# Optimization experiments

Hardware: AMD Instinct MI355X
Metric: run time of the kernel (lower is better)

## Reference

```python
import math
import jax, jax.numpy as jnp
import numpy as np

B, T, E, H = 4, 4096, 512, 8
D = E // H
TOP_K = int(3 * math.log(T))  # autocorrelation_factor * log(time_length) = 24


def setup_inputs() -> dict:
    key = jax.random.key(0)
    ks = jax.random.split(key, 9)
    s = 0.02
    return {
        "hidden_states": jax.random.normal(ks[0], (B, T, E), jnp.float32),
        "Wq": jax.random.normal(ks[1], (E, E), jnp.float32) * s,
        "bq": jax.random.normal(ks[2], (E,), jnp.float32) * s,
        "Wk": jax.random.normal(ks[3], (E, E), jnp.float32) * s,
        "bk": jax.random.normal(ks[4], (E,), jnp.float32) * s,
        "Wv": jax.random.normal(ks[5], (E, E), jnp.float32) * s,
        "bv": jax.random.normal(ks[6], (E,), jnp.float32) * s,
        "Wo": jax.random.normal(ks[7], (E, E), jnp.float32) * s,
        "bo": jax.random.normal(ks[8], (E,), jnp.float32) * s,
    }


def _heads(x):
    # [B,T,E] -> [B*H,T,D] (b-major over heads, matching torch view/transpose/reshape)
    return x.reshape(B, T, H, D).transpose(0, 2, 1, 3).reshape(B * H, T, D)


def reference(hidden_states, Wq, bq, Wk, bk, Wv, bv, Wo, bo):
    q = _heads(hidden_states @ Wq.T + bq)
    k = _heads(hidden_states @ Wk.T + bk)
    v = _heads(hidden_states @ Wv.T + bv)

    # FFT-based autocorrelation: irfft(rfft(q) * conj(rfft(k)))  -> [B*H,T,D]
    qf = jnp.fft.rfft(q, n=T, axis=1)
    kf = jnp.fft.rfft(k, n=T, axis=1)
    ac = jnp.fft.irfft(qf * jnp.conj(kf), n=T, axis=1)

    # mean over heads and channels -> [B,T]; eval-mode per-batch top-k delays
    ac_mean = ac.reshape(B, H, T, D).mean(axis=(1, 3))
    top_vals, top_idx = jax.lax.top_k(ac_mean, TOP_K)      # [B,K]
    w = jax.nn.softmax(top_vals, axis=-1)                  # [B,K]

    # torch .repeat(num_heads,...) tiles batch entries: row j uses batch j % B
    w_t = jnp.tile(w, (H, 1))        # [B*H,K]
    d_t = jnp.tile(top_idx, (H, 1))  # [B*H,K]

    t = jnp.arange(T)
    agg = jnp.zeros_like(v)
    for i in range(TOP_K):
        idx = (t[None, :] + d_t[:, i:i + 1]) % T           # circular shift by -delay
        rolled = jnp.take_along_axis(v, idx[:, :, None], axis=1)
        agg = agg + w_t[:, i][:, None, None] * rolled

    out = agg.reshape(B, H, T, D).transpose(0, 2, 1, 3).reshape(B, T, E)
    return out @ Wo.T + bo
```

## Files before the change

kernel.cpp:

```cpp
#include <hip/hip_runtime.h>
#include <math.h>

#define B_ 4
#define T_ 4096
#define E_ 512
#define H_ 8
#define TOPK 24
#define FH 2049
#define FHP 2064

typedef __attribute__((ext_vector_type(8))) short bf16x8;
typedef __attribute__((ext_vector_type(4))) float f32x4;

__device__ __forceinline__ unsigned short f2bf(float f) {
    unsigned u = __float_as_uint(f);
    u = (u + 0x7FFFu + ((u >> 16) & 1u)) >> 16;
    return (unsigned short)u;
}
__device__ __forceinline__ float bf2f(unsigned short h) {
    return __uint_as_float(((unsigned)h) << 16);
}

__global__ __launch_bounds__(256) void split_hidden(const float* __restrict__ x,
                                                    unsigned short* __restrict__ hi,
                                                    unsigned short* __restrict__ lo)
{
    int i = (blockIdx.x * 256 + threadIdx.x) * 4;
    float4 v = *(const float4*)&x[i];
    float f[4] = {v.x, v.y, v.z, v.w};
    unsigned short hh[4], ll[4];
#pragma unroll
    for (int j = 0; j < 4; j++) {
        hh[j] = f2bf(f[j]);
        ll[j] = f2bf(f[j] - bf2f(hh[j]));
    }
    *(ushort4*)&hi[i] = make_ushort4(hh[0], hh[1], hh[2], hh[3]);
    *(ushort4*)&lo[i] = make_ushort4(ll[0], ll[1], ll[2], ll[3]);
}

__global__ __launch_bounds__(256) void split_w4(const float* __restrict__ w0,
                                                const float* __restrict__ w1,
                                                const float* __restrict__ w2,
                                                const float* __restrict__ w3,
                                                unsigned short* __restrict__ hi,
                                                unsigned short* __restrict__ lo)
{
    const float* src = (blockIdx.y == 0) ? w0 : (blockIdx.y == 1) ? w1
                     : (blockIdx.y == 2) ? w2 : w3;
    size_t off = (size_t)blockIdx.y * (E_ * E_);
    int i = (blockIdx.x * 256 + threadIdx.x) * 4;
    float4 v = *(const float4*)&src[i];
    float f[4] = {v.x, v.y, v.z, v.w};
    unsigned short hh[4], ll[4];
#pragma unroll
    for (int j = 0; j < 4; j++) {
        hh[j] = f2bf(f[j]);
        ll[j] = f2bf(f[j] - bf2f(hh[j]));
    }
    *(ushort4*)&hi[off + i] = make_ushort4(hh[0], hh[1], hh[2], hh[3]);
    *(ushort4*)&lo[off + i] = make_ushort4(ll[0], ll[1], ll[2], ll[3]);
}

template<int PASSES, int OMODE>
__global__ __launch_bounds__(256) void mfma_gemm(const unsigned short* __restrict__ Ah,
                                                 const unsigned short* __restrict__ Al,
                                                 const unsigned short* __restrict__ Bh,
                                                 const unsigned short* __restrict__ Bl,
                                                 const float* __restrict__ bias,
                                                 const float* __restrict__ bias2,
                                                 void* __restrict__ Cp)
{
    constexpr int NT = (PASSES == 3) ? 4 : 2;
    constexpr int TSZ = 128 * 40;
    __shared__ short smem[NT * TSZ];
    const int tid = threadIdx.x;
    const int m0 = blockIdx.x * 128;
    const int n0 = blockIdx.y * 128;
    const int wid = tid >> 6, lane = tid & 63;
    const int wn = wid >> 1, wm = wid & 1;
    const int lr = lane & 15, lg = lane >> 4;
    const int kb = lg * 8;

    short* At  = smem;
    short* Alt = smem + ((PASSES == 3) ? TSZ : 0);
    short* Bt  = smem + ((PASSES == 3) ? 2 : 1) * TSZ;
    short* Blt = smem + ((PASSES == 3) ? 3 : 1) * TSZ;

    f32x4 acc[4][4];
#pragma unroll
    for (int i = 0; i < 4; i++)
#pragma unroll
        for (int j = 0; j < 4; j++) acc[i][j] = (f32x4)0.f;

    const int c0 = tid, c1 = tid + 256;
    const int r0 = c0 >> 2, kp0 = (c0 & 3) << 3;
    const int r1 = c1 >> 2, kp1 = (c1 & 3) << 3;

    for (int k0 = 0; k0 < 512; k0 += 32) {
        __syncthreads();
        *(bf16x8*)&At[r0 * 40 + kp0] = *(const bf16x8*)&Ah[(size_t)(n0 + r0) * 512 + k0 + kp0];
        *(bf16x8*)&At[r1 * 40 + kp1] = *(const bf16x8*)&Ah[(size_t)(n0 + r1) * 512 + k0 + kp1];
        *(bf16x8*)&Bt[r0 * 40 + kp0] = *(const bf16x8*)&Bh[(size_t)(m0 + r0) * 512 + k0 + kp0];
        *(bf16x8*)&Bt[r1 * 40 + kp1] = *(const bf16x8*)&Bh[(size_t)(m0 + r1) * 512 + k0 + kp1];
        if (PASSES == 3) {
            *(bf16x8*)&Alt[r0 * 40 + kp0] = *(const bf16x8*)&Al[(size_t)(n0 + r0) * 512 + k0 + kp0];
            *(bf16x8*)&Alt[r1 * 40 + kp1] = *(const bf16x8*)&Al[(size_t)(n0 + r1) * 512 + k0 + kp1];
            *(bf16x8*)&Blt[r0 * 40 + kp0] = *(const bf16x8*)&Bl[(size_t)(m0 + r0) * 512 + k0 + kp0];
            *(bf16x8*)&Blt[r1 * 40 + kp1] = *(const bf16x8*)&Bl[(size_t)(m0 + r1) * 512 + k0 + kp1];
        }
        __syncthreads();
        bf16x8 a[4], b[4];
#pragma unroll
        for (int f = 0; f < 4; f++) {
            a[f] = *(bf16x8*)&At[(wn * 64 + f * 16 + lr) * 40 + kb];
            b[f] = *(bf16x8*)&Bt[(wm * 64 + f * 16 + lr) * 40 + kb];
        }
        if (PASSES == 3) {
            bf16x8 a2[4], b2[4];
#pragma unroll
            for (int f = 0; f < 4; f++) {
                a2[f] = *(bf16x8*)&Alt[(wn * 64 + f * 16 + lr) * 40 + kb];
                b2[f] = *(bf16x8*)&Blt[(wm * 64 + f * 16 + lr) * 40 + kb];
            }
#pragma unroll
            for (int i = 0; i < 4; i++)
#pragma unroll
                for (int j = 0; j < 4; j++) {
                    acc[i][j] = __builtin_amdgcn_mfma_f32_16x16x32_bf16(a[i], b[j], acc[i][j], 0, 0, 0);
                    acc[i][j] = __builtin_amdgcn_mfma_f32_16x16x32_bf16(a[i], b2[j], acc[i][j], 0, 0, 0);
                    acc[i][j] = __builtin_amdgcn_mfma_f32_16x16x32_bf16(a2[i], b[j], acc[i][j], 0, 0, 0);
                }
        } else {
#pragma unroll
            for (int i = 0; i < 4; i++)
#pragma unroll
                for (int j = 0; j < 4; j++)
                    acc[i][j] = __builtin_amdgcn_mfma_f32_16x16x32_bf16(a[i], b[j], acc[i][j], 0, 0, 0);
        }
    }

    const float* bp = (m0 >= 512) ? bias2 : bias;
    const int mb = m0 & 511;
    float bs[4];
#pragma unroll
    for (int j = 0; j < 4; j++) bs[j] = bp[mb + wm * 64 + j * 16 + lr];

    if (OMODE == 1) {
        float* C = (float*)Cp;
        const int qk = m0 >> 9;
        const int bidx = n0 >> 12;
        const int t0 = (n0 & 4095) + wn * 64;
#pragma unroll
        for (int i = 0; i < 4; i++)
#pragma unroll
            for (int j = 0; j < 4; j++) {
                int t = t0 + i * 16 + lg * 4;
                int e = mb + wm * 64 + j * 16 + lr;
                size_t row = (size_t)(qk * 2048 + bidx * 512 + e);
                float4 o = make_float4(acc[i][j][0] + bs[j], acc[i][j][1] + bs[j],
                                       acc[i][j][2] + bs[j], acc[i][j][3] + bs[j]);
                *(float4*)&C[row * 4096 + t] = o;
            }
    } else if (OMODE == 0) {
        float* C = (float*)Cp;
#pragma unroll
        for (int i = 0; i < 4; i++)
#pragma unroll
            for (int j = 0; j < 4; j++) {
                int m = m0 + wm * 64 + j * 16 + lr;
#pragma unroll
                for (int r = 0; r < 4; r++) {
                    int n = n0 + wn * 64 + i * 16 + lg * 4 + r;
                    C[(size_t)n * 512 + m] = acc[i][j][r] + bs[j];
                }
            }
    } else {
        unsigned short* C = (unsigned short*)Cp;
#pragma unroll
        for (int i = 0; i < 4; i++)
#pragma unroll
            for (int j = 0; j < 4; j++) {
                int m = m0 + wm * 64 + j * 16 + lr;
#pragma unroll
                for (int r = 0; r < 4; r++) {
                    int n = n0 + wn * 64 + i * 16 + lg * 4 + r;
                    C[(size_t)n * 512 + m] = f2bf(acc[i][j][r] + bs[j]);
                }
            }
    }
}

template<int SGN>
__device__ __forceinline__ void radix8(float* xr, float* xi)
{
    const float C = 0.70710678118654752440f;
    const float S = (float)SGN;
    float t0r = xr[0] + xr[4], t0i = xi[0] + xi[4];
    float t1r = xr[1] + xr[5], t1i = xi[1] + xi[5];
    float t2r = xr[2] + xr[6], t2i = xi[2] + xi[6];
    float t3r = xr[3] + xr[7], t3i = xi[3] + xi[7];
    float u0r = xr[0] - xr[4], u0i = xi[0] - xi[4];
    float a1r = xr[1] - xr[5], a1i = xi[1] - xi[5];
    float a2r = xr[2] - xr[6], a2i = xi[2] - xi[6];
    float a3r = xr[3] - xr[7], a3i = xi[3] - xi[7];
    float u1r = C * (a1r - S * a1i), u1i = C * (S * a1r + a1i);
    float u2r = -S * a2i,            u2i = S * a2r;
    float u3r = -C * (a3r + S * a3i), u3i = C * (S * a3r - a3i);
    float v0r = t0r + t2r, v0i = t0i + t2i;
    float w0r = t0r - t2r, w0i = t0i - t2i;
    float v1r = t1r + t3r, v1i = t1i + t3i;
    float w1r = -S * (t1i - t3i), w1i = S * (t1r - t3r);
    float p0r = u0r + u2r, p0i = u0i + u2i;
    float q0r = u0r - u2r, q0i = u0i - u2i;
    float p1r = u1r + u3r, p1i = u1i + u3i;
    float q1r = -S * (u1i - u3i), q1i = S * (u1r - u3r);
    xr[0] = v0r + v1r; xi[0] = v0i + v1i;
    xr[4] = v0r - v1r; xi[4] = v0i - v1i;
    xr[2] = w0r + w1r; xi[2] = w0i + w1i;
    xr[6] = w0r - w1r; xi[6] = w0i - w1i;
    xr[1] = p0r + p1r; xi[1] = p0i + p1i;
    xr[5] = p0r - p1r; xi[5] = p0i - p1i;
    xr[3] = q0r + q1r; xi[3] = q0i + q1i;
    xr[7] = q0r - q1r; xi[7] = q0i - q1i;
}

__device__ __forceinline__ void twmul(float& xr, float& xi, float wc, float ws)
{
    float a = xr, b = xi;
    xr = a * wc - b * ws;
    xi = a * ws + b * wc;
}

__device__ __forceinline__ void twiddle7(float* xr, float* xi, int n, float ang)
{
    float s1, c1;
    __sincosf(ang * (float)n, &s1, &c1);
    float wc = c1, ws = s1;
    twmul(xr[1], xi[1], wc, ws);
#pragma unroll
    for (int r = 2; r < 8; r++) {
        float nc = wc * c1 - ws * s1;
        float ns = wc * s1 + ws * c1;
        wc = nc; ws = ns;
        twmul(xr[r], xi[r], wc, ws);
    }
}

#define SW(i) ((i) + ((i) >> 3))

template<int SGN>
__device__ __forceinline__ void fft_core(float* xr, float* xi,
                                         float* lre, float* lim, int tid)
{
    const float TW = (float)SGN * 6.28318530717958647693f;
    __syncthreads();
    radix8<SGN>(xr, xi);
    twiddle7(xr, xi, tid, TW / 4096.f);
#pragma unroll
    for (int r = 0; r < 8; r++) {
        int idx = r * 512 + tid;
        lre[SW(idx)] = xr[r]; lim[SW(idx)] = xi[r];
    }
    __syncthreads();
    const int b2 = (tid >> 6) * 512, n2 = tid & 63;
#pragma unroll
    for (int s = 0; s < 8; s++) {
        int idx = b2 + n2 + s * 64;
        xr[s] = lre[SW(idx)]; xi[s] = lim[SW(idx)];
    }
    __syncthreads();
    radix8<SGN>(xr, xi);
    twiddle7(xr, xi, n2, TW / 512.f);
#pragma unroll
    for (int r = 0; r < 8; r++) {
        int idx = b2 + r * 64 + n2;
        lre[SW(idx)] = xr[r]; lim[SW(idx)] = xi[r];
    }
    __syncthreads();
    const int b3 = (tid >> 3) * 64, n3 = tid & 7;
#pragma unroll
    for (int s = 0; s < 8; s++) {
        int idx = b3 + n3 + s * 8;
        xr[s] = lre[SW(idx)]; xi[s] = lim[SW(idx)];
    }
    __syncthreads();
    radix8<SGN>(xr, xi);
    twiddle7(xr, xi, n3, TW / 64.f);
#pragma unroll
    for (int r = 0; r < 8; r++) {
        int idx = b3 + r * 8 + n3;
        lre[SW(idx)] = xr[r]; lim[SW(idx)] = xi[r];
    }
    __syncthreads();
#pragma unroll
    for (int s = 0; s < 8; s++) {
        int idx = tid * 8 + s;
        xr[s] = lre[SW(idx)]; xi[s] = lim[SW(idx)];
    }
    __syncthreads();
    radix8<SGN>(xr, xi);
    const int fr = ((tid & 7) << 6) | (((tid >> 3) & 7) << 3) | (tid >> 6);
#pragma unroll
    for (int r = 0; r < 8; r++) {
        int f = r * 512 + fr;
        lre[SW(f)] = xr[r]; lim[SW(f)] = xi[r];
    }
    __syncthreads();
}

__global__ __launch_bounds__(512) void fft_fwd_kernel(const float* __restrict__ Qt,
                                                      const float* __restrict__ Kt,
                                                      float2* __restrict__ prodp)
{
    __shared__ float lre[4608];
    __shared__ float lim[4608];
    const int bid = blockIdx.x;
    const int tid = threadIdx.x;
    const int b = bid >> 7, chunk = bid & 127;
    float par[5] = {0.f, 0.f, 0.f, 0.f, 0.f};
    float pai[4] = {0.f, 0.f, 0.f, 0.f};
    for (int c = 0; c < 4; c++) {
        const int e = chunk * 4 + c;
        const float* q = Qt + ((size_t)(b * 512 + e)) * 4096;
        const float* k = Kt + ((size_t)(b * 512 + e)) * 4096;
        float xr[8], xi[8];
#pragma unroll
        for (int s = 0; s < 8; s++) {
            xr[s] = q[tid + 512 * s];
            xi[s] = k[tid + 512 * s];
        }
        fft_core<-1>(xr, xi, lre, lim, tid);
#pragma unroll
        for (int s = 0; s < 4; s++) {
            int f = tid + 512 * s;
            int nf = (4096 - f) & 4095;
            float Ax = lre[SW(f)],  Ay = lim[SW(f)];
            float Bx = lre[SW(nf)], By = lim[SW(nf)];
            float qx = 0.5f * (Ax + Bx), qy = 0.5f * (Ay - By);
            float kx = 0.5f * (Ay + By), ky = -0.5f * (Ax - Bx);
            par[s] += qx * kx + qy * ky;
            pai[s] += qy * kx - qx * ky;
        }
        if (tid == 0) {
            float Ax = lre[SW(2048)], Ay = lim[SW(2048)];
            par[4] += Ax * Ay;
        }
    }
    float2* out = prodp + (size_t)bid * FHP;
#pragma unroll
    for (int s = 0; s < 4; s++)
        out[tid + 512 * s] = make_float2(par[s], pai[s]);
    if (tid == 0) out[2048] = make_float2(par[4], 0.f);
}

__global__ __launch_bounds__(256) void reduce_s(const float2* __restrict__ prodp,
                                                float2* __restrict__ S)
{
    const int f = blockIdx.x * 256 + threadIdx.x;
    const int b = blockIdx.y;
    if (f >= FH) return;
    float sx = 0.f, sy = 0.f;
    const float2* p = prodp + (size_t)(b * 128) * FHP + f;
#pragma unroll 8
    for (int j = 0; j < 128; j++) {
        float2 v = p[(size_t)j * FHP];
        sx += v.x; sy += v.y;
    }
    S[b * FHP + f] = make_float2(sx, sy);
}

__global__ __launch_bounds__(512) void ifft_kernel(const float2* __restrict__ S,
                                                   float* __restrict__ acm)
{
    __shared__ float lre[4608];
    __shared__ float lim[4608];
    const int b = blockIdx.x, tid = threadIdx.x;
    float xr[8], xi[8];
#pragma unroll
    for (int s = 0; s < 8; s++) {
        int idx = tid + 512 * s;
        if (idx <= 2048) {
            float2 v = S[b * FHP + idx];
            xr[s] = v.x; xi[s] = v.y;
        } else {
            float2 v = S[b * FHP + (4096 - idx)];
            xr[s] = v.x; xi[s] = -v.y;
        }
    }
    fft_core<1>(xr, xi, lre, lim, tid);
    const float scale = 1.0f / ((float)T_ * (float)E_);
#pragma unroll
    for (int s = 0; s < 8; s++) {
        int p = tid + 512 * s;
        acm[b * T_ + p] = lre[SW(p)] * scale;
    }
}

__global__ __launch_bounds__(256) void topk_kernel(const float* __restrict__ acm,
                                                   int* __restrict__ delays,
                                                   float* __restrict__ weights)
{
    __shared__ float vals[4096];
    __shared__ float bv[256];
    __shared__ int   bi[256];
    __shared__ float topv[TOPK];
    const int b = blockIdx.x, tid = threadIdx.x;
#pragma unroll
    for (int s = 0; s < 16; s++) vals[tid + 256 * s] = acm[b * T_ + tid + 256 * s];
    __syncthreads();
    for (int it = 0; it < TOPK; it++) {
        float best = -INFINITY; int bidx = 0;
#pragma unroll
        for (int s = 0; s < 16; s++) {
            int idx = tid * 16 + s;
            float v = vals[idx];
            if (v > best) { best = v; bidx = idx; }
        }
        bv[tid] = best; bi[tid] = bidx;
        __syncthreads();
        for (int off = 128; off > 0; off >>= 1) {
            if (tid < off) {
                if (bv[tid + off] > bv[tid] ||
                    (bv[tid + off] == bv[tid] && bi[tid + off] < bi[tid])) {
                    bv[tid] = bv[tid + off]; bi[tid] = bi[tid + off];
                }
            }
            __syncthreads();
        }
        if (tid == 0) {
            delays[b * TOPK + it] = bi[0];
            topv[it] = bv[0];
            vals[bi[0]] = -INFINITY;
        }
        __syncthreads();
    }
    if (tid == 0) {
        float mx = topv[0];
        float w[TOPK], sum = 0.f;
        for (int i = 0; i < TOPK; i++) { w[i] = expf(topv[i] - mx); sum += w[i]; }
        for (int i = 0; i < TOPK; i++) weights[b * TOPK + i] = w[i] / sum;
    }
}

__global__ __launch_bounds__(256) void agg_kernel(const unsigned short* __restrict__ V,
                                                  const int* __restrict__ delays,
                                                  const float* __restrict__ wts,
                                                  unsigned short* __restrict__ agg)
{
    __shared__ int   dly[B_][TOPK];
    __shared__ float wt[B_][TOPK];
    const int tid = threadIdx.x, b = blockIdx.y;
    if (tid < B_ * TOPK) {
        dly[tid / TOPK][tid % TOPK] = delays[tid];
        wt[tid / TOPK][tid % TOPK]  = wts[tid];
    }
    __syncthreads();
    const int lane = tid & 63, w = tid >> 6;
    const int t = blockIdx.x * 4 + w;
    const int e8 = lane * 8;
    const int h = e8 >> 6;
    const int c = (b * H_ + h) % B_;
    const unsigned short* Vb = V + (size_t)b * T_ * E_;
    float acc[8];
#pragma unroll
    for (int j = 0; j < 8; j++) acc[j] = 0.f;
#pragma unroll
    for (int i = 0; i < TOPK; i++) {
        int tt = (t + dly[c][i]) & (T_ - 1);
        bf16x8 v = *(const bf16x8*)&Vb[(size_t)tt * E_ + e8];
        float wg = wt[c][i];
#pragma unroll
        for (int j = 0; j < 8; j++)
            acc[j] += wg * bf2f((unsigned short)v[j]);
    }
    bf16x8 o;
#pragma unroll
    for (int j = 0; j < 8; j++) o[j] = (short)f2bf(acc[j]);
    *(bf16x8*)&agg[((size_t)b * T_ + t) * E_ + e8] = o;
}

extern "C" void kernel_launch(void* const* d_in, const int* in_sizes, int n_in,
                              void* d_out, int out_size, void* d_ws, size_t ws_size,
                              hipStream_t stream)
{
    const float* hidden = (const float*)d_in[0];
    const float* Wq = (const float*)d_in[1]; const float* bq = (const float*)d_in[2];
    const float* Wk = (const float*)d_in[3]; const float* bk = (const float*)d_in[4];
    const float* Wv = (const float*)d_in[5]; const float* bv = (const float*)d_in[6];
    const float* Wo = (const float*)d_in[7]; const float* bo = (const float*)d_in[8];

    char* ws = (char*)d_ws;
    const size_t QT_OFF  = 0;
    const size_t KT_OFF  = 33554432;
    const size_t VB_OFF  = 67108864;
    const size_t BIG_OFF = 83886080;
    const size_t BIG2_OFF= 100663296;
    const size_t WHI_OFF = 117702656;
    const size_t WLO_OFF = 119799808;
    const size_t S_OFF   = 121896960;
    const size_t ACM_OFF = 121963008;
    const size_t DEL_OFF = 122028544;
    const size_t WTS_OFF = 122028928;
    if (ws_size < 122029312) return;

    float*  Qt   = (float*)(ws + QT_OFF);
    unsigned short* Vb  = (unsigned short*)(ws + VB_OFF);
    unsigned short* Ah  = (unsigned short*)(ws + BIG_OFF);
    unsigned short* Al  = (unsigned short*)(ws + BIG2_OFF);
    float2* prodp = (float2*)(ws + BIG_OFF);
    unsigned short* Ag  = (unsigned short*)(ws + BIG2_OFF);
    unsigned short* Whi = (unsigned short*)(ws + WHI_OFF);
    unsigned short* Wlo = (unsigned short*)(ws + WLO_OFF);
    float2* S    = (float2*)(ws + S_OFF);
    float*  acm  = (float*)(ws + ACM_OFF);
    int*    delays = (int*)(ws + DEL_OFF);
    float*  wts    = (float*)(ws + WTS_OFF);

    unsigned short* Wvh = Whi + 2 * 262144;
    unsigned short* Woh = Whi + 3 * 262144;

    split_hidden<<<8192, 256, 0, stream>>>(hidden, Ah, Al);
    dim3 wg(256, 4);
    split_w4<<<wg, 256, 0, stream>>>(Wq, Wk, Wv, Wo, Whi, Wlo);

    dim3 gqk(8, 128);
    mfma_gemm<3, 1><<<gqk, 256, 0, stream>>>(Ah, Al, Whi, Wlo, bq, bk, Qt);
    dim3 gv(4, 128);
    mfma_gemm<1, 2><<<gv, 256, 0, stream>>>(Ah, Ah, Wvh, Wvh, bv, bv, Vb);

    fft_fwd_kernel<<<512, 512, 0, stream>>>(Qt, (float*)(ws + KT_OFF), prodp);
    dim3 rg((FH + 255) / 256, B_);
    reduce_s<<<rg, 256, 0, stream>>>(prodp, S);
    ifft_kernel<<<B_, 512, 0, stream>>>(S, acm);
    topk_kernel<<<B_, 256, 0, stream>>>(acm, delays, wts);

    dim3 ag(T_ / 4, B_);
    agg_kernel<<<ag, 256, 0, stream>>>(Vb, delays, wts, Ag);
    mfma_gemm<1, 0><<<gv, 256, 0, stream>>>(Ag, Ag, Woh, Woh, bo, bo, (float*)d_out);
}
```

Baseline: 231.3 us.

## FFT hidden states directly and fold Wq/Wk into one precomputed bilinear matrix

The Q and K projections followed by two FFTs are replaced by one FFT of the transposed hidden states (linearity). The cross-spectrum sum is then computed as a bilinear form using M = Wq^T·Wk, which is formed per call and split into bf16 hi/lo parts. A 3-pass split-bf16 MFMA GEMM produces Y = Z·M, and a dot kernel reduces Y against Z per frequency. The q/k biases are dropped, since they only change the DC bin and so only add a constant to the autocorrelation, which top-k and softmax ignore. This removes the 1024-wide QK projection, halves the number of FFT rows and cuts the fp32 workspace traffic, at the cost of a new transpose kernel, the M-prep GEMM and extra bf16 split error on the spectra.

```diff
diff --git a/kernel.cpp b/kernel.cpp
--- a/kernel.cpp
+++ b/kernel.cpp
@@ -8,6 +8,8 @@
 #define TOPK 24
 #define FH 2049
 #define FHP 2064
+#define F2 2064
+#define ZROWS 16512
 
 typedef __attribute__((ext_vector_type(8))) short bf16x8;
 typedef __attribute__((ext_vector_type(4))) float f32x4;
@@ -21,53 +23,110 @@
     return __uint_as_float(((unsigned)h) << 16);
 }
 
-__global__ __launch_bounds__(256) void split_hidden(const float* __restrict__ x,
-                                                    unsigned short* __restrict__ hi,
-                                                    unsigned short* __restrict__ lo)
-{
-    int i = (blockIdx.x * 256 + threadIdx.x) * 4;
-    float4 v = *(const float4*)&x[i];
-    float f[4] = {v.x, v.y, v.z, v.w};
-    unsigned short hh[4], ll[4];
-#pragma unroll
-    for (int j = 0; j < 4; j++) {
-        hh[j] = f2bf(f[j]);
-        ll[j] = f2bf(f[j] - bf2f(hh[j]));
-    }
-    *(ushort4*)&hi[i] = make_ushort4(hh[0], hh[1], hh[2], hh[3]);
-    *(ushort4*)&lo[i] = make_ushort4(ll[0], ll[1], ll[2], ll[3]);
-}
-
-__global__ __launch_bounds__(256) void split_w4(const float* __restrict__ w0,
-                                                const float* __restrict__ w1,
-                                                const float* __restrict__ w2,
-                                                const float* __restrict__ w3,
-                                                unsigned short* __restrict__ hi,
-                                                unsigned short* __restrict__ lo)
-{
-    const float* src = (blockIdx.y == 0) ? w0 : (blockIdx.y == 1) ? w1
-                     : (blockIdx.y == 2) ? w2 : w3;
-    size_t off = (size_t)blockIdx.y * (E_ * E_);
+__global__ __launch_bounds__(256) void trsp_split(const float* __restrict__ hid,
+                                                  float* __restrict__ Htr,
+                                                  unsigned short* __restrict__ Ah)
+{
+    __shared__ float tile[64][68];
+    const int b = blockIdx.z;
+    const int t0 = blockIdx.x * 64, e0 = blockIdx.y * 64;
+    const int r = threadIdx.x >> 4;
+    const int c4 = (threadIdx.x & 15) * 4;
+#pragma unroll
+    for (int s = 0; s < 4; s++) {
+        int t = t0 + r + 16 * s;
+        float4 v = *(const float4*)&hid[((size_t)b * T_ + t) * E_ + e0 + c4];
+        tile[r + 16 * s][c4 + 0] = v.x; tile[r + 16 * s][c4 + 1] = v.y;
+        tile[r + 16 * s][c4 + 2] = v.z; tile[r + 16 * s][c4 + 3] = v.w;
+        ushort4 hv = make_ushort4(f2bf(v.x), f2bf(v.y), f2bf(v.z), f2bf(v.w));
+        *(ushort4*)&Ah[((size_t)b * T_ + t) * E_ + e0 + c4] = hv;
+    }
+    __syncthreads();
+#pragma unroll
+    for (int s = 0; s < 4; s++) {
+        int e = e0 + r + 16 * s;
+        float4 o;
+        o.x = tile[c4 + 0][r + 16 * s];
+        o.y = tile[c4 + 1][r + 16 * s];
+        o.z = tile[c4 + 2][r + 16 * s];
+        o.w = tile[c4 + 3][r + 16 * s];
+        *(float4*)&Htr[((size_t)b * E_ + e) * T_ + t0 + c4] = o;
+    }
+}
+
+__global__ __launch_bounds__(256) void split_w2(const float* __restrict__ wv,
+                                                const float* __restrict__ wo,
+                                                unsigned short* __restrict__ Wvh,
+                                                unsigned short* __restrict__ Woh)
+{
+    const float* src = blockIdx.y ? wo : wv;
+    unsigned short* dst = blockIdx.y ? Woh : Wvh;
     int i = (blockIdx.x * 256 + threadIdx.x) * 4;
     float4 v = *(const float4*)&src[i];
-    float f[4] = {v.x, v.y, v.z, v.w};
-    unsigned short hh[4], ll[4];
-#pragma unroll
-    for (int j = 0; j < 4; j++) {
-        hh[j] = f2bf(f[j]);
-        ll[j] = f2bf(f[j] - bf2f(hh[j]));
-    }
-    *(ushort4*)&hi[off + i] = make_ushort4(hh[0], hh[1], hh[2], hh[3]);
-    *(ushort4*)&lo[off + i] = make_ushort4(ll[0], ll[1], ll[2], ll[3]);
-}
-
-template<int PASSES, int OMODE>
+    *(ushort4*)&dst[i] = make_ushort4(f2bf(v.x), f2bf(v.y), f2bf(v.z), f2bf(v.w));
+}
+
+__global__ __launch_bounds__(256) void wprep_m(const float* __restrict__ Wq,
+                                               const float* __restrict__ Wk,
+                                               unsigned short* __restrict__ Mth,
+                                               unsigned short* __restrict__ Mtl)
+{
+    __shared__ float As[8][132];
+    __shared__ float Bs[8][132];
+    const int j0 = blockIdx.x * 128, k0 = blockIdx.y * 128;
+    const int tid = threadIdx.x;
+    const int tm = tid & 15, tn = tid >> 4;
+    const int le = tid >> 5, lc = (tid & 31) * 4;
+    float acc[8][8];
+#pragma unroll
+    for (int i = 0; i < 8; i++)
+#pragma unroll
+        for (int j = 0; j < 8; j++) acc[i][j] = 0.f;
+    for (int eb = 0; eb < 512; eb += 8) {
+        __syncthreads();
+        *(float4*)&As[le][lc] = *(const float4*)&Wq[((size_t)(eb + le)) * 512 + k0 + lc];
+        *(float4*)&Bs[le][lc] = *(const float4*)&Wk[((size_t)(eb + le)) * 512 + j0 + lc];
+        __syncthreads();
+#pragma unroll
+        for (int e = 0; e < 8; e++) {
+            float a[8], bb[8];
+            *(float4*)&a[0] = *(float4*)&As[e][4 * tn];
+            *(float4*)&a[4] = *(float4*)&As[e][64 + 4 * tn];
+            *(float4*)&bb[0] = *(float4*)&Bs[e][4 * tm];
+            *(float4*)&bb[4] = *(float4*)&Bs[e][64 + 4 * tm];
+#pragma unroll
+            for (int i = 0; i < 8; i++)
+#pragma unroll
+                for (int j = 0; j < 8; j++)
+                    acc[i][j] += a[i] * bb[j];
+        }
+    }
+#pragma unroll
+    for (int jj = 0; jj < 8; jj++) {
+        int j = j0 + ((jj < 4) ? (4 * tm + jj) : (64 + 4 * tm + jj - 4));
+        ushort4 h0, l0, h1, l1;
+        float v0[4] = {acc[0][jj], acc[1][jj], acc[2][jj], acc[3][jj]};
+        float v1[4] = {acc[4][jj], acc[5][jj], acc[6][jj], acc[7][jj]};
+        unsigned short hh[4], ll[4];
+#pragma unroll
+        for (int r = 0; r < 4; r++) { hh[r] = f2bf(v0[r]); ll[r] = f2bf(v0[r] - bf2f(hh[r])); }
+        h0 = make_ushort4(hh[0], hh[1], hh[2], hh[3]); l0 = make_ushort4(ll[0], ll[1], ll[2], ll[3]);
+#pragma unroll
+        for (int r = 0; r < 4; r++) { hh[r] = f2bf(v1[r]); ll[r] = f2bf(v1[r] - bf2f(hh[r])); }
+        h1 = make_ushort4(hh[0], hh[1], hh[2], hh[3]); l1 = make_ushort4(ll[0], ll[1], ll[2], ll[3]);
+        *(ushort4*)&Mth[(size_t)j * 512 + k0 + 4 * tn] = h0;
+        *(ushort4*)&Mtl[(size_t)j * 512 + k0 + 4 * tn] = l0;
+        *(ushort4*)&Mth[(size_t)j * 512 + k0 + 64 + 4 * tn] = h1;
+        *(ushort4*)&Mtl[(size_t)j * 512 + k0 + 64 + 4 * tn] = l1;
+    }
+}
+
+template<int PASSES, int AMODE, int OMODE, int HASBIAS>
 __global__ __launch_bounds__(256) void mfma_gemm(const unsigned short* __restrict__ Ah,
                                                  const unsigned short* __restrict__ Al,
                                                  const unsigned short* __restrict__ Bh,
                                                  const unsigned short* __restrict__ Bl,
                                                  const float* __restrict__ bias,
-                                                 const float* __restrict__ bias2,
                                                  void* __restrict__ Cp)
 {
     constexpr int NT = (PASSES == 3) ? 4 : 2;
@@ -92,19 +151,26 @@
 #pragma unroll
         for (int j = 0; j < 4; j++) acc[i][j] = (f32x4)0.f;
 
-    const int c0 = tid, c1 = tid + 256;
-    const int r0 = c0 >> 2, kp0 = (c0 & 3) << 3;
-    const int r1 = c1 >> 2, kp1 = (c1 & 3) << 3;
+    const int r0 = tid >> 2, kp0 = (tid & 3) << 3;
+    const int r1 = (tid + 256) >> 2, kp1 = ((tid + 256) & 3) << 3;
 
     for (int k0 = 0; k0 < 512; k0 += 32) {
         __syncthreads();
-        *(bf16x8*)&At[r0 * 40 + kp0] = *(const bf16x8*)&Ah[(size_t)(n0 + r0) * 512 + k0 + kp0];
-        *(bf16x8*)&At[r1 * 40 + kp1] = *(const bf16x8*)&Ah[(size_t)(n0 + r1) * 512 + k0 + kp1];
+        size_t a0, a1;
+        if (AMODE == 0) {
+            a0 = (size_t)(n0 + r0) * 512 + k0 + kp0;
+            a1 = (size_t)(n0 + r1) * 512 + k0 + kp1;
+        } else {
+            a0 = ((size_t)((k0 + kp0) >> 3) * ZROWS + n0 + r0) * 8;
+            a1 = ((size_t)((k0 + kp1) >> 3) * ZROWS + n0 + r1) * 8;
+        }
+        *(bf16x8*)&At[r0 * 40 + kp0] = *(const bf16x8*)&Ah[a0];
+        *(bf16x8*)&At[r1 * 40 + kp1] = *(const bf16x8*)&Ah[a1];
         *(bf16x8*)&Bt[r0 * 40 + kp0] = *(const bf16x8*)&Bh[(size_t)(m0 + r0) * 512 + k0 + kp0];
         *(bf16x8*)&Bt[r1 * 40 + kp1] = *(const bf16x8*)&Bh[(size_t)(m0 + r1) * 512 + k0 + kp1];
         if (PASSES == 3) {
-            *(bf16x8*)&Alt[r0 * 40 + kp0] = *(const bf16x8*)&Al[(size_t)(n0 + r0) * 512 + k0 + kp0];
-            *(bf16x8*)&Alt[r1 * 40 + kp1] = *(const bf16x8*)&Al[(size_t)(n0 + r1) * 512 + k0 + kp1];
+            *(bf16x8*)&Alt[r0 * 40 + kp0] = *(const bf16x8*)&Al[a0];
+            *(bf16x8*)&Alt[r1 * 40 + kp1] = *(const bf16x8*)&Al[a1];
             *(bf16x8*)&Blt[r0 * 40 + kp0] = *(const bf16x8*)&Bl[(size_t)(m0 + r0) * 512 + k0 + kp0];
             *(bf16x8*)&Blt[r1 * 40 + kp1] = *(const bf16x8*)&Bl[(size_t)(m0 + r1) * 512 + k0 + kp1];
         }
@@ -139,29 +205,11 @@
         }
     }
 
-    const float* bp = (m0 >= 512) ? bias2 : bias;
-    const int mb = m0 & 511;
     float bs[4];
 #pragma unroll
-    for (int j = 0; j < 4; j++) bs[j] = bp[mb + wm * 64 + j * 16 + lr];
-
-    if (OMODE == 1) {
-        float* C = (float*)Cp;
-        const int qk = m0 >> 9;
-        const int bidx = n0 >> 12;
-        const int t0 = (n0 & 4095) + wn * 64;
-#pragma unroll
-        for (int i = 0; i < 4; i++)
-#pragma unroll
-            for (int j = 0; j < 4; j++) {
-                int t = t0 + i * 16 + lg * 4;
-                int e = mb + wm * 64 + j * 16 + lr;
-                size_t row = (size_t)(qk * 2048 + bidx * 512 + e);
-                float4 o = make_float4(acc[i][j][0] + bs[j], acc[i][j][1] + bs[j],
-                                       acc[i][j][2] + bs[j], acc[i][j][3] + bs[j]);
-                *(float4*)&C[row * 4096 + t] = o;
-            }
-    } else if (OMODE == 0) {
+    for (int j = 0; j < 4; j++) bs[j] = HASBIAS ? bias[m0 + wm * 64 + j * 16 + lr] : 0.f;
+
+    if (OMODE == 0) {
         float* C = (float*)Cp;
 #pragma unroll
         for (int i = 0; i < 4; i++)
@@ -204,7 +252,7 @@
     float a2r = xr[2] - xr[6], a2i = xi[2] - xi[6];
     float a3r = xr[3] - xr[7], a3i = xi[3] - xi[7];
     float u1r = C * (a1r - S * a1i), u1i = C * (S * a1r + a1i);
-    float u2r = -S * a2i,            u2i = S * a2r;
+    float u2r = -S * a2i,             u2i = S * a2r;
     float u3r = -C * (a3r + S * a3i), u3i = C * (S * a3r - a3i);
     float v0r = t0r + t2r, v0i = t0i + t2i;
     float w0r = t0r - t2r, w0i = t0i - t2i;
@@ -308,26 +356,26 @@
     __syncthreads();
 }
 
-__global__ __launch_bounds__(512) void fft_fwd_kernel(const float* __restrict__ Qt,
-                                                      const float* __restrict__ Kt,
-                                                      float2* __restrict__ prodp)
+__global__ __launch_bounds__(512) void fft_fwd_z(const float* __restrict__ Htr,
+                                                 unsigned short* __restrict__ Zh,
+                                                 unsigned short* __restrict__ Zl)
 {
     __shared__ float lre[4608];
     __shared__ float lim[4608];
     const int bid = blockIdx.x;
     const int tid = threadIdx.x;
-    const int b = bid >> 7, chunk = bid & 127;
-    float par[5] = {0.f, 0.f, 0.f, 0.f, 0.f};
-    float pai[4] = {0.f, 0.f, 0.f, 0.f};
-    for (int c = 0; c < 4; c++) {
-        const int e = chunk * 4 + c;
-        const float* q = Qt + ((size_t)(b * 512 + e)) * 4096;
-        const float* k = Kt + ((size_t)(b * 512 + e)) * 4096;
+    const int b = bid >> 6, g = bid & 63;
+    const int e0 = g * 8;
+    unsigned uh[4][2][4], ul[4][2][4];
+#pragma unroll
+    for (int p = 0; p < 4; p++) {
+        const float* he = Htr + ((size_t)(b * 512 + e0 + 2 * p)) * 4096;
+        const float* ho = Htr + ((size_t)(b * 512 + e0 + 2 * p + 1)) * 4096;
         float xr[8], xi[8];
 #pragma unroll
         for (int s = 0; s < 8; s++) {
-            xr[s] = q[tid + 512 * s];
-            xi[s] = k[tid + 512 * s];
+            xr[s] = he[tid + 512 * s];
+            xi[s] = ho[tid + 512 * s];
         }
         fft_core<-1>(xr, xi, lre, lim, tid);
 #pragma unroll
@@ -338,35 +386,79 @@
             float Bx = lre[SW(nf)], By = lim[SW(nf)];
             float qx = 0.5f * (Ax + Bx), qy = 0.5f * (Ay - By);
             float kx = 0.5f * (Ay + By), ky = -0.5f * (Ax - Bx);
-            par[s] += qx * kx + qy * ky;
-            pai[s] += qy * kx - qx * ky;
+            unsigned short h0 = f2bf(qx), h1 = f2bf(kx);
+            unsigned short l0 = f2bf(qx - bf2f(h0)), l1 = f2bf(kx - bf2f(h1));
+            uh[s][0][p] = (unsigned)h0 | ((unsigned)h1 << 16);
+            ul[s][0][p] = (unsigned)l0 | ((unsigned)l1 << 16);
+            unsigned short h2 = f2bf(qy), h3 = f2bf(ky);
+            unsigned short l2 = f2bf(qy - bf2f(h2)), l3 = f2bf(ky - bf2f(h3));
+            uh[s][1][p] = (unsigned)h2 | ((unsigned)h3 << 16);
+            ul[s][1][p] = (unsigned)l2 | ((unsigned)l3 << 16);
         }
         if (tid == 0) {
             float Ax = lre[SW(2048)], Ay = lim[SW(2048)];
-            par[4] += Ax * Ay;
-        }
-    }
-    float2* out = prodp + (size_t)bid * FHP;
+            size_t r2048 = ((size_t)b * F2 + 2048) * 2;
+            size_t base0 = ((size_t)g * ZROWS + r2048) * 8 + 2 * p;
+            unsigned short h = f2bf(Ax);
+            Zh[base0] = h; Zl[base0] = f2bf(Ax - bf2f(h));
+            unsigned short h2 = f2bf(Ay);
+            Zh[base0 + 1] = h2; Zl[base0 + 1] = f2bf(Ay - bf2f(h2));
+            size_t base1 = ((size_t)g * ZROWS + r2048 + 1) * 8 + 2 * p;
+            Zh[base1] = 0; Zl[base1] = 0;
+            Zh[base1 + 1] = 0; Zl[base1 + 1] = 0;
+        }
+    }
 #pragma unroll
     for (int s = 0; s < 4; s++)
-        out[tid + 512 * s] = make_float2(par[s], pai[s]);
-    if (tid == 0) out[2048] = make_float2(par[4], 0.f);
-}
-
-__global__ __launch_bounds__(256) void reduce_s(const float2* __restrict__ prodp,
-                                                float2* __restrict__ S)
-{
-    const int f = blockIdx.x * 256 + threadIdx.x;
+#pragma unroll
+        for (int c = 0; c < 2; c++) {
+            size_t row = ((size_t)b * F2 + tid + 512 * s) * 2 + c;
+            size_t off = ((size_t)g * ZROWS + row) * 8;
+            bf16x8 vh, vl;
+#pragma unroll
+            for (int p = 0; p < 4; p++) {
+                vh[2 * p]     = (short)(uh[s][c][p] & 0xffff);
+                vh[2 * p + 1] = (short)(uh[s][c][p] >> 16);
+                vl[2 * p]     = (short)(ul[s][c][p] & 0xffff);
+                vl[2 * p + 1] = (short)(ul[s][c][p] >> 16);
+            }
+            *(bf16x8*)&Zh[off] = vh;
+            *(bf16x8*)&Zl[off] = vl;
+        }
+}
+
+__global__ __launch_bounds__(256) void dot_s(const float* __restrict__ Y,
+                                             const unsigned short* __restrict__ Zh,
+                                             const unsigned short* __restrict__ Zl,
+                                             float2* __restrict__ S)
+{
+    const int lane = threadIdx.x & 63, w = threadIdx.x >> 6;
+    const int f = blockIdx.x * 256 + w * 64 + lane;
     const int b = blockIdx.y;
-    if (f >= FH) return;
-    float sx = 0.f, sy = 0.f;
-    const float2* p = prodp + (size_t)(b * 128) * FHP + f;
-#pragma unroll 8
-    for (int j = 0; j < 128; j++) {
-        float2 v = p[(size_t)j * FHP];
-        sx += v.x; sy += v.y;
-    }
-    S[b * FHP + f] = make_float2(sx, sy);
+    if (f > 2048) return;
+    const size_t row = ((size_t)b * F2 + f) * 2;
+    float sre = 0.f, sim = 0.f;
+    for (int g = 0; g < 64; g++) {
+        size_t zoff = ((size_t)g * ZROWS + row) * 8;
+        bf16x8 zrh = *(const bf16x8*)&Zh[zoff];
+        bf16x8 zrl = *(const bf16x8*)&Zl[zoff];
+        bf16x8 zih = *(const bf16x8*)&Zh[zoff + 8];
+        bf16x8 zil = *(const bf16x8*)&Zl[zoff + 8];
+        const float* yr = &Y[row * 512 + g * 8];
+        const float* yi = &Y[(row + 1) * 512 + g * 8];
+        float4 yr0 = *(const float4*)yr,       yr1 = *(const float4*)(yr + 4);
+        float4 yi0 = *(const float4*)yi,       yi1 = *(const float4*)(yi + 4);
+        float yrv[8] = {yr0.x, yr0.y, yr0.z, yr0.w, yr1.x, yr1.y, yr1.z, yr1.w};
+        float yiv[8] = {yi0.x, yi0.y, yi0.z, yi0.w, yi1.x, yi1.y, yi1.z, yi1.w};
+#pragma unroll
+        for (int j = 0; j < 8; j++) {
+            float zr = bf2f((unsigned short)zrh[j]) + bf2f((unsigned short)zrl[j]);
+            float zi = bf2f((unsigned short)zih[j]) + bf2f((unsigned short)zil[j]);
+            sre += yrv[j] * zr + yiv[j] * zi;
+            sim += yiv[j] * zr - yrv[j] * zi;
+        }
+    }
+    S[b * FHP + f] = make_float2(sre, sim);
 }
 
 __global__ __launch_bounds__(512) void ifft_kernel(const float2* __restrict__ S,
@@ -484,57 +576,64 @@
                               hipStream_t stream)
 {
     const float* hidden = (const float*)d_in[0];
-    const float* Wq = (const float*)d_in[1]; const float* bq = (const float*)d_in[2];
-    const float* Wk = (const float*)d_in[3]; const float* bk = (const float*)d_in[4];
+    const float* Wq = (const float*)d_in[1];
+    const float* Wk = (const float*)d_in[3];
     const float* Wv = (const float*)d_in[5]; const float* bv = (const float*)d_in[6];
     const float* Wo = (const float*)d_in[7]; const float* bo = (const float*)d_in[8];
 
     char* ws = (char*)d_ws;
-    const size_t QT_OFF  = 0;
-    const size_t KT_OFF  = 33554432;
-    const size_t VB_OFF  = 67108864;
-    const size_t BIG_OFF = 83886080;
-    const size_t BIG2_OFF= 100663296;
-    const size_t WHI_OFF = 117702656;
-    const size_t WLO_OFF = 119799808;
-    const size_t S_OFF   = 121896960;
-    const size_t ACM_OFF = 121963008;
-    const size_t DEL_OFF = 122028544;
-    const size_t WTS_OFF = 122028928;
-    if (ws_size < 122029312) return;
-
-    float*  Qt   = (float*)(ws + QT_OFF);
+    const size_t YA_OFF  = 0;
+    const size_t AH_OFF  = 33816576;
+    const size_t ZH_OFF  = 50593792;
+    const size_t ZL_OFF  = 67502080;
+    const size_t VB_OFF  = 84410368;
+    const size_t MTH_OFF = 101187584;
+    const size_t MTL_OFF = 101711872;
+    const size_t WVH_OFF = 102236160;
+    const size_t WOH_OFF = 102760448;
+    const size_t S_OFF   = 103284736;
+    const size_t ACM_OFF = 103350784;
+    const size_t DEL_OFF = 103416320;
+    const size_t WTS_OFF = 103416704;
+    if (ws_size < 103417088) return;
+
+    float* Htr = (float*)(ws + YA_OFF);
+    float* Y   = (float*)(ws + YA_OFF);
+    unsigned short* Ah  = (unsigned short*)(ws + AH_OFF);
+    unsigned short* Ag  = (unsigned short*)(ws + AH_OFF);
+    unsigned short* Zh  = (unsigned short*)(ws + ZH_OFF);
+    unsigned short* Zl  = (unsigned short*)(ws + ZL_OFF);
     unsigned short* Vb  = (unsigned short*)(ws + VB_OFF);
-    unsigned short* Ah  = (unsigned short*)(ws + BIG_OFF);
-    unsigned short* Al  = (unsigned short*)(ws + BIG2_OFF);
-    float2* prodp = (float2*)(ws + BIG_OFF);
-    unsigned short* Ag  = (unsigned short*)(ws + BIG2_OFF);
-    unsigned short* Whi = (unsigned short*)(ws + WHI_OFF);
-    unsigned short* Wlo = (unsigned short*)(ws + WLO_OFF);
+    unsigned short* Mth = (unsigned short*)(ws + MTH_OFF);
+    unsigned short* Mtl = (unsigned short*)(ws + MTL_OFF);
+    unsigned short* Wvh = (unsigned short*)(ws + WVH_OFF);
+    unsigned short* Woh = (unsigned short*)(ws + WOH_OFF);
     float2* S    = (float2*)(ws + S_OFF);
     float*  acm  = (float*)(ws + ACM_OFF);
     int*    delays = (int*)(ws + DEL_OFF);
     float*  wts    = (float*)(ws + WTS_OFF);
 
-    unsigned short* Wvh = Whi + 2 * 262144;
-    unsigned short* Woh = Whi + 3 * 262144;
-
-    split_hidden<<<8192, 256, 0, stream>>>(hidden, Ah, Al);
-    dim3 wg(256, 4);
-    split_w4<<<wg, 256, 0, stream>>>(Wq, Wk, Wv, Wo, Whi, Wlo);
-
-    dim3 gqk(8, 128);
-    mfma_gemm<3, 1><<<gqk, 256, 0, stream>>>(Ah, Al, Whi, Wlo, bq, bk, Qt);
+    dim3 tg(64, 8, 4);
+    trsp_split<<<tg, 256, 0, stream>>>(hidden, Htr, Ah);
+    dim3 swg(256, 2);
+    split_w2<<<swg, 256, 0, stream>>>(Wv, Wo, Wvh, Woh);
+    dim3 mg(4, 4);
+    wprep_m<<<mg, 256, 0, stream>>>(Wq, Wk, Mth, Mtl);
+
     dim3 gv(4, 128);
-    mfma_gemm<1, 2><<<gv, 256, 0, stream>>>(Ah, Ah, Wvh, Wvh, bv, bv, Vb);
-
-    fft_fwd_kernel<<<512, 512, 0, stream>>>(Qt, (float*)(ws + KT_OFF), prodp);
-    dim3 rg((FH + 255) / 256, B_);
-    reduce_s<<<rg, 256, 0, stream>>>(prodp, S);
+    mfma_gemm<1, 0, 2, 1><<<gv, 256, 0, stream>>>(Ah, Ah, Wvh, Wvh, bv, Vb);
+
+    fft_fwd_z<<<256, 512, 0, stream>>>(Htr, Zh, Zl);
+
+    dim3 gy(4, 129);
+    mfma_gemm<3, 1, 0, 0><<<gy, 256, 0, stream>>>(Zh, Zl, Mth, Mtl, bv, Y);
+
+    dim3 dg(9, 4);
+    dot_s<<<dg, 256, 0, stream>>>(Y, Zh, Zl, S);
+
     ifft_kernel<<<B_, 512, 0, stream>>>(S, acm);
     topk_kernel<<<B_, 256, 0, stream>>>(acm, delays, wts);
-
     dim3 ag(T_ / 4, B_);
     agg_kernel<<<ag, 256, 0, stream>>>(Vb, delays, wts, Ag);
-    mfma_gemm<1, 0><<<gv, 256, 0, stream>>>(Ag, Ag, Woh, Woh, bo, bo, (float*)d_out);
-}
+    mfma_gemm<1, 0, 0, 1><<<gv, 256, 0, stream>>>(Ag, Ag, Woh, Woh, bo, (float*)d_out);
+}
```

After: 342.9 us. 1.48x slower.
